# Optimization experiments

Hardware: AMD Instinct MI355X
Metric: run time of the kernel (lower is better)

## Reference

```python
import jax, jax.numpy as jnp
import numpy as np

EPS = 1e-5

def _layernorm(x, g, b):
    mu = x.mean(-1, keepdims=True)
    var = ((x - mu) ** 2).mean(-1, keepdims=True)
    return (x - mu) * jax.lax.rsqrt(var + EPS) * g + b

def setup_inputs() -> dict:
    key = jax.random.key(0)
    ks = jax.random.split(key, 8)
    T, TOK, E = 16, 16384, 128
    N_NODE, NUM_NODES = 8192, 50000
    COMP_LEN, MAX_LEN, COMP_DIM = 64, 782, 32
    return {
        "x": jax.random.normal(ks[0], (T, TOK, E), jnp.float32),
        "ln1_g": jax.random.normal(ks[1], (E,), jnp.float32),
        "ln1_b": jax.random.normal(ks[2], (E,), jnp.float32),
        "ln2_g": jax.random.normal(ks[3], (COMP_LEN * COMP_DIM,), jnp.float32),
        "ln2_b": jax.random.normal(ks[4], (COMP_LEN * COMP_DIM,), jnp.float32),
        "node_idx": jax.random.randint(ks[5], (T, N_NODE), 0, NUM_NODES),
        "stacked_indices": jax.random.randint(ks[6], (COMP_LEN, MAX_LEN), 0, NUM_NODES),
        "n_node": N_NODE,
        "num_nodes": NUM_NODES,
    }

def reference(x, ln1_g, ln1_b, ln2_g, ln2_b, node_idx, stacked_indices, n_node, num_nodes):
    T, TOK, E = x.shape
    comp_len, max_len = stacked_indices.shape
    comp_dim = ln2_g.shape[0] // comp_len
    # encode_layer_norm over embed_dim
    xn = _layernorm(x, ln1_g, ln1_b)
    # node tokens occupy the first n_node token slots (padded_node_mask)
    nodes = xn[:, :n_node, :]                              # [T, n_node, E]
    # scga._to_entire: scatter-add per-timestamp node embeds to entire-node tensor
    flat_idx = (jnp.arange(T)[:, None] * num_nodes + node_idx).reshape(-1)
    tee = jax.ops.segment_sum(nodes.reshape(-1, E), flat_idx,
                              num_segments=T * num_nodes)
    tee = tee.reshape(T, num_nodes, E)                     # [T, N, E]
    # AdaptiveAvgPool1d(comp_dim): exact block mean since E % comp_dim == 0
    pooled = tee.reshape(T, num_nodes, comp_dim, E // comp_dim).mean(-1)  # [T, N, C]
    # basket gather + mean over basket slots
    gath = pooled[:, stacked_indices, :]                   # [T, comp_len, max_len, C]
    agg = gath.sum(2) / max_len                            # [T, comp_len, C]
    compressed = agg.reshape(T, 1, comp_len * comp_dim)
    return _layernorm(compressed, ln2_g, ln2_b)
```

## Files before the change

kernel.cpp:

```cpp
#include <hip/hip_runtime.h>
#include <hip/hip_cooperative_groups.h>

namespace cg = cooperative_groups;

constexpr int T_DIM       = 16;
constexpr int TOK         = 16384;
constexpr int E_DIM       = 128;
constexpr int N_NODE_C    = 8192;
constexpr int NUM_NODES_C = 50000;
constexpr int COMP_LEN_C  = 64;
constexpr int MAX_LEN_C   = 782;
constexpr int COMP_DIM_C  = 32;
constexpr float EPS_F     = 1e-5f;

constexpr int D2      = COMP_LEN_C * COMP_DIM_C;
constexpr int GRID_C  = 1024;
constexpr int BLK_C   = 256;
constexpr int PER_T   = 64;
constexpr int RPB     = 128;
constexpr int W_WORDS = NUM_NODES_C * COMP_LEN_C / 4;

constexpr size_t W8_BYTES = (size_t)NUM_NODES_C * COMP_LEN_C;
constexpr size_t P_OFF    = 3211264;
constexpr size_t AGG_OFF  = P_OFF + (size_t)T_DIM * PER_T * D2 * 4;

struct SharedT {
  float    vtile[RPB][COMP_DIM_C];
  unsigned atile[RPB][16];
  float    red[256];
};

__device__ __forceinline__ void phase_main(
    SharedT& sh, int bid, const float* __restrict__ x, const float* __restrict__ g1,
    const float* __restrict__ b1, const int* __restrict__ node_idx,
    const unsigned* __restrict__ W32, float* __restrict__ P) {
  const int t = bid >> 6, chunk = bid & 63;
  const int tid = threadIdx.x, lane = tid & 63, wave = tid >> 6;
  const int g = lane & 31, half = lane >> 5;
  const int rbase = chunk * RPB;
  const int* nit = node_idx + (size_t)t * N_NODE_C;
  const float4* xv = reinterpret_cast<const float4*>(x + (size_t)t * TOK * E_DIM);

  int nid8[8];
#pragma unroll
  for (int j = 0; j < 8; ++j) nid8[j] = nit[rbase + ((tid + j * 256) >> 4)];

  const float4 gv = *reinterpret_cast<const float4*>(g1 + g * 4);
  const float4 bv = *reinterpret_cast<const float4*>(b1 + g * 4);
  const float sg = gv.x + gv.y + gv.z + gv.w;
  const float sb = bv.x + bv.y + bv.z + bv.w;
  const int wr0 = rbase + wave * 32;

  float4 xd[8];
#pragma unroll
  for (int i = 0; i < 8; ++i)
    xd[i] = xv[(size_t)(wr0 + 2 * i) * 32 + lane];

  unsigned wg8[8];
#pragma unroll
  for (int j = 0; j < 8; ++j)
    wg8[j] = W32[(size_t)nid8[j] * 16 + ((tid + j * 256) & 15)];

#pragma unroll
  for (int i = 0; i < 8; ++i) {
    const float4 a = xd[i];
    float s = (a.x + a.y) + (a.z + a.w);
    float q = a.x * a.x + a.y * a.y + a.z * a.z + a.w * a.w;
#pragma unroll
    for (int m = 1; m < 32; m <<= 1) { s += __shfl_xor(s, m); q += __shfl_xor(q, m); }
    float mu = s * (1.0f / E_DIM);
    float rstd = rsqrtf(q * (1.0f / E_DIM) - mu * mu + EPS_F);
    float dxg = a.x * gv.x + a.y * gv.y + a.z * gv.z + a.w * gv.w;
    sh.vtile[wave * 32 + 2 * i + half][g] = (dxg - mu * sg) * rstd + sb;
  }
#pragma unroll
  for (int i = 0; i < 8; ++i)
    xd[i] = xv[(size_t)(wr0 + 16 + 2 * i) * 32 + lane];
#pragma unroll
  for (int j = 0; j < 8; ++j) {
    int w = tid + j * 256;
    sh.atile[w >> 4][w & 15] = wg8[j];
  }
#pragma unroll
  for (int i = 0; i < 8; ++i) {
    const float4 a = xd[i];
    float s = (a.x + a.y) + (a.z + a.w);
    float q = a.x * a.x + a.y * a.y + a.z * a.z + a.w * a.w;
#pragma unroll
    for (int m = 1; m < 32; m <<= 1) { s += __shfl_xor(s, m); q += __shfl_xor(q, m); }
    float mu = s * (1.0f / E_DIM);
    float rstd = rsqrtf(q * (1.0f / E_DIM) - mu * mu + EPS_F);
    float dxg = a.x * gv.x + a.y * gv.y + a.z * gv.z + a.w * gv.w;
    sh.vtile[wave * 32 + 16 + 2 * i + half][g] = (dxg - mu * sg) * rstd + sb;
  }
  __syncthreads();

  const int c4 = tid >> 4, d2 = tid & 15;
  float2 acc0{0,0}, acc1{0,0}, acc2{0,0}, acc3{0,0};
  const float2* vt2 = reinterpret_cast<const float2*>(&sh.vtile[0][0]);
#pragma unroll 4
  for (int k = 0; k < RPB; ++k) {
    unsigned a4 = sh.atile[k][c4];
    float2 v2 = vt2[k * 16 + d2];
    float a0 = (float)(a4 & 255u),         a1 = (float)((a4 >> 8) & 255u);
    float a2 = (float)((a4 >> 16) & 255u), a3 = (float)((a4 >> 24) & 255u);
    acc0.x += a0 * v2.x; acc0.y += a0 * v2.y;
    acc1.x += a1 * v2.x; acc1.y += a1 * v2.y;
    acc2.x += a2 * v2.x; acc2.y += a2 * v2.y;
    acc3.x += a3 * v2.x; acc3.y += a3 * v2.y;
  }
  float2* pr2 = reinterpret_cast<float2*>(P + ((size_t)t * PER_T + chunk) * D2);
  pr2[(c4 * 4 + 0) * 16 + d2] = acc0;
  pr2[(c4 * 4 + 1) * 16 + d2] = acc1;
  pr2[(c4 * 4 + 2) * 16 + d2] = acc2;
  pr2[(c4 * 4 + 3) * 16 + d2] = acc3;
}

__device__ __forceinline__ void phase_reduce(
    SharedT& sh, int b, const float* __restrict__ P, float* __restrict__ Agg) {
  const int t = b >> 5, seg = b & 31;
  const int tid = threadIdx.x;
  const int elem = seg * 64 + (tid & 63);
  const int q = tid >> 6;
  const float* base = P + (size_t)t * PER_T * D2 + elem;
  float acc = 0.f;
#pragma unroll
  for (int p = 0; p < 16; ++p) acc += base[(size_t)(q * 16 + p) * D2];
  sh.red[tid] = acc;
  __syncthreads();
  if (tid < 64)
    Agg[(size_t)t * D2 + elem] =
        sh.red[tid] + sh.red[tid + 64] + sh.red[tid + 128] + sh.red[tid + 192];
}

__device__ __forceinline__ void phase_final(
    SharedT& sh, int t, const float* __restrict__ Agg, const float* __restrict__ g2,
    const float* __restrict__ b2, float* __restrict__ out) {
  const float scale = 1.0f / (4.0f * (float)MAX_LEN_C);
  const int tid = threadIdx.x;
  float y[8]; float s = 0.f, q = 0.f;
#pragma unroll
  for (int k = 0; k < 8; ++k) {
    float v = Agg[(size_t)t * D2 + tid * 8 + k] * scale;
    y[k] = v; s += v; q += v * v;
  }
#pragma unroll
  for (int m = 1; m < 64; m <<= 1) { s += __shfl_xor(s, m); q += __shfl_xor(q, m); }
  const int w = tid >> 6, ln = tid & 63;
  if (ln == 0) { sh.red[w] = s; sh.red[8 + w] = q; }
  __syncthreads();
  float ts = sh.red[0] + sh.red[1] + sh.red[2] + sh.red[3];
  float tq = sh.red[8] + sh.red[9] + sh.red[10] + sh.red[11];
  float mu = ts * (1.0f / D2);
  float rstd = rsqrtf(tq * (1.0f / D2) - mu * mu + EPS_F);
#pragma unroll
  for (int k = 0; k < 8; ++k) {
    int idx = tid * 8 + k;
    out[(size_t)t * D2 + idx] = (y[k] - mu) * rstd * g2[idx] + b2[idx];
  }
}

__global__ __launch_bounds__(256, 4) void mega_kernel(
    const float* __restrict__ x, const float* __restrict__ g1, const float* __restrict__ b1,
    const int* __restrict__ node_idx, const int* __restrict__ sidx,
    const float* __restrict__ g2, const float* __restrict__ b2,
    unsigned* __restrict__ W8w, float* __restrict__ P, float* __restrict__ Agg,
    float* __restrict__ out) {
  cg::grid_group grid = cg::this_grid();
  __shared__ SharedT sh;
  const int gtid = blockIdx.x * BLK_C + threadIdx.x;

  for (int i = gtid; i < W_WORDS; i += GRID_C * BLK_C) W8w[i] = 0u;
  grid.sync();
  if (gtid < COMP_LEN_C * MAX_LEN_C) {
    int c = gtid / MAX_LEN_C;
    int n = sidx[gtid];
    int byteoff = n * COMP_LEN_C + c;
    atomicAdd(&W8w[byteoff >> 2], 1u << (8 * (byteoff & 3)));
  }
  grid.sync();
  phase_main(sh, blockIdx.x, x, g1, b1, node_idx, (const unsigned*)W8w, P);
  grid.sync();
  if (blockIdx.x < 512) phase_reduce(sh, blockIdx.x, P, Agg);
  grid.sync();
  if (blockIdx.x < T_DIM) phase_final(sh, blockIdx.x, Agg, g2, b2, out);
}

__global__ void build_w8_kernel(const int* __restrict__ sidx, unsigned* __restrict__ W8w) {
  const int c  = blockIdx.x >> 2;
  const int jc = blockIdx.x & 3;
  const int j  = jc * 196 + threadIdx.x;
  if (j < MAX_LEN_C && threadIdx.x < 196) {
    int n = sidx[c * MAX_LEN_C + j];
    int byteoff = n * COMP_LEN_C + c;
    atomicAdd(&W8w[byteoff >> 2], 1u << (8 * (byteoff & 3)));
  }
}
__global__ __launch_bounds__(256, 4) void main_nc(
    const float* __restrict__ x, const float* __restrict__ g1, const float* __restrict__ b1,
    const int* __restrict__ node_idx, const unsigned* __restrict__ W32,
    float* __restrict__ P) {
  __shared__ SharedT sh;
  phase_main(sh, blockIdx.x, x, g1, b1, node_idx, W32, P);
}
__global__ __launch_bounds__(256) void reduce_nc(const float* __restrict__ P,
                                                float* __restrict__ Agg) {
  __shared__ SharedT sh;
  phase_reduce(sh, blockIdx.x, P, Agg);
}
__global__ __launch_bounds__(256) void final_nc(
    const float* __restrict__ Agg, const float* __restrict__ g2,
    const float* __restrict__ b2, float* __restrict__ out) {
  __shared__ SharedT sh;
  phase_final(sh, blockIdx.x, Agg, g2, b2, out);
}

extern "C" void kernel_launch(void* const* d_in, const int* in_sizes, int n_in,
                              void* d_out, int out_size, void* d_ws, size_t ws_size,
                              hipStream_t stream) {
  const float* x     = (const float*)d_in[0];
  const float* ln1_g = (const float*)d_in[1];
  const float* ln1_b = (const float*)d_in[2];
  const float* ln2_g = (const float*)d_in[3];
  const float* ln2_b = (const float*)d_in[4];
  const int* node_idx = (const int*)d_in[5];
  const int* sidx     = (const int*)d_in[6];
  float* out = (float*)d_out;

  unsigned char* ws = (unsigned char*)d_ws;
  unsigned* W8w = (unsigned*)ws;
  float* P   = (float*)(ws + P_OFF);
  float* Agg = (float*)(ws + AGG_OFF);

  int maxActive = 0;
  hipError_t occ = hipOccupancyMaxActiveBlocksPerMultiprocessor(
      &maxActive, (const void*)mega_kernel, BLK_C, 0);
  bool coop = (occ == hipSuccess) && (maxActive >= 4);

  if (coop) {
    void* args[] = {(void*)&x, (void*)&ln1_g, (void*)&ln1_b, (void*)&node_idx,
                    (void*)&sidx, (void*)&ln2_g, (void*)&ln2_b,
                    (void*)&W8w, (void*)&P, (void*)&Agg, (void*)&out};
    hipError_t e = hipLaunchCooperativeKernel((void*)mega_kernel, dim3(GRID_C),
                                              dim3(BLK_C), args, 0, stream);
    if (e == hipSuccess) return;
  }

  hipMemsetAsync(W8w, 0, W8_BYTES, stream);
  build_w8_kernel<<<COMP_LEN_C * 4, 256, 0, stream>>>(sidx, W8w);
  main_nc<<<GRID_C, BLK_C, 0, stream>>>(x, ln1_g, ln1_b, node_idx,
                                        (const unsigned*)W8w, P);
  reduce_nc<<<512, 256, 0, stream>>>(P, Agg);
  final_nc<<<T_DIM, 256, 0, stream>>>(Agg, ln2_g, ln2_b, out);
}
```

Measured before the change: 43.46 us.

## Overlap LN streaming with weight build, atomically accumulate partials, drop reduce phase

The layernorm streaming of x now runs before the first grid sync, so it overlaps with building the basket count table. Per-block partial sums are added straight into the per-timestamp aggregate with float atomics, which removes the partial buffer, the separate reduce phase and one grid sync. Zeroing of the count table and aggregate moves from in-kernel stores to a host-issued memset before the launch. The cost is atomic contention (64 blocks per timestamp add into the same 2048 floats), nondeterministic float summation order, and an extra memset operation on the stream.

```diff
diff --git a/kernel.cpp b/kernel.cpp
--- a/kernel.cpp
+++ b/kernel.cpp
@@ -18,30 +18,28 @@
 constexpr int BLK_C   = 256;
 constexpr int PER_T   = 64;
 constexpr int RPB     = 128;
-constexpr int W_WORDS = NUM_NODES_C * COMP_LEN_C / 4;
-
-constexpr size_t W8_BYTES = (size_t)NUM_NODES_C * COMP_LEN_C;
-constexpr size_t P_OFF    = 3211264;
-constexpr size_t AGG_OFF  = P_OFF + (size_t)T_DIM * PER_T * D2 * 4;
+
+constexpr size_t W8_BYTES   = (size_t)NUM_NODES_C * COMP_LEN_C;
+constexpr size_t AGG_OFF    = 3211264;
+constexpr size_t AGG_BYTES  = (size_t)T_DIM * D2 * sizeof(float);
+constexpr size_t ZERO_BYTES = AGG_OFF + AGG_BYTES;
 
 struct SharedT {
   float    vtile[RPB][COMP_DIM_C];
   unsigned atile[RPB][16];
-  float    red[256];
+  float    red[16];
 };
 
-__device__ __forceinline__ void phase_main(
-    SharedT& sh, int bid, const float* __restrict__ x, const float* __restrict__ g1,
-    const float* __restrict__ b1, const int* __restrict__ node_idx,
-    const unsigned* __restrict__ W32, float* __restrict__ P) {
-  const int t = bid >> 6, chunk = bid & 63;
+__device__ __forceinline__ void phaseA_stream(
+    SharedT& sh, int t, int chunk, const float* __restrict__ x,
+    const float* __restrict__ g1, const float* __restrict__ b1,
+    const int* __restrict__ node_idx, int* nid8) {
   const int tid = threadIdx.x, lane = tid & 63, wave = tid >> 6;
   const int g = lane & 31, half = lane >> 5;
   const int rbase = chunk * RPB;
   const int* nit = node_idx + (size_t)t * N_NODE_C;
   const float4* xv = reinterpret_cast<const float4*>(x + (size_t)t * TOK * E_DIM);
 
-  int nid8[8];
 #pragma unroll
   for (int j = 0; j < 8; ++j) nid8[j] = nit[rbase + ((tid + j * 256) >> 4)];
 
@@ -55,12 +53,6 @@
 #pragma unroll
   for (int i = 0; i < 8; ++i)
     xd[i] = xv[(size_t)(wr0 + 2 * i) * 32 + lane];
-
-  unsigned wg8[8];
-#pragma unroll
-  for (int j = 0; j < 8; ++j)
-    wg8[j] = W32[(size_t)nid8[j] * 16 + ((tid + j * 256) & 15)];
-
 #pragma unroll
   for (int i = 0; i < 8; ++i) {
     const float4 a = xd[i];
@@ -77,11 +69,6 @@
   for (int i = 0; i < 8; ++i)
     xd[i] = xv[(size_t)(wr0 + 16 + 2 * i) * 32 + lane];
 #pragma unroll
-  for (int j = 0; j < 8; ++j) {
-    int w = tid + j * 256;
-    sh.atile[w >> 4][w & 15] = wg8[j];
-  }
-#pragma unroll
   for (int i = 0; i < 8; ++i) {
     const float4 a = xd[i];
     float s = (a.x + a.y) + (a.z + a.w);
@@ -92,6 +79,23 @@
     float rstd = rsqrtf(q * (1.0f / E_DIM) - mu * mu + EPS_F);
     float dxg = a.x * gv.x + a.y * gv.y + a.z * gv.z + a.w * gv.w;
     sh.vtile[wave * 32 + 16 + 2 * i + half][g] = (dxg - mu * sg) * rstd + sb;
+  }
+}
+
+__device__ __forceinline__ void phaseB_gemmflush(
+    SharedT& sh, int t, const unsigned* __restrict__ W32, const int* nid8,
+    float* __restrict__ Agg) {
+  const int tid = threadIdx.x;
+  __syncthreads();
+
+  unsigned wg8[8];
+#pragma unroll
+  for (int j = 0; j < 8; ++j)
+    wg8[j] = W32[(size_t)nid8[j] * 16 + ((tid + j * 256) & 15)];
+#pragma unroll
+  for (int j = 0; j < 8; ++j) {
+    int w = tid + j * 256;
+    sh.atile[w >> 4][w & 15] = wg8[j];
   }
   __syncthreads();
 
@@ -109,31 +113,19 @@
     acc2.x += a2 * v2.x; acc2.y += a2 * v2.y;
     acc3.x += a3 * v2.x; acc3.y += a3 * v2.y;
   }
-  float2* pr2 = reinterpret_cast<float2*>(P + ((size_t)t * PER_T + chunk) * D2);
-  pr2[(c4 * 4 + 0) * 16 + d2] = acc0;
-  pr2[(c4 * 4 + 1) * 16 + d2] = acc1;
-  pr2[(c4 * 4 + 2) * 16 + d2] = acc2;
-  pr2[(c4 * 4 + 3) * 16 + d2] = acc3;
-}
-
-__device__ __forceinline__ void phase_reduce(
-    SharedT& sh, int b, const float* __restrict__ P, float* __restrict__ Agg) {
-  const int t = b >> 5, seg = b & 31;
-  const int tid = threadIdx.x;
-  const int elem = seg * 64 + (tid & 63);
-  const int q = tid >> 6;
-  const float* base = P + (size_t)t * PER_T * D2 + elem;
-  float acc = 0.f;
-#pragma unroll
-  for (int p = 0; p < 16; ++p) acc += base[(size_t)(q * 16 + p) * D2];
-  sh.red[tid] = acc;
-  __syncthreads();
-  if (tid < 64)
-    Agg[(size_t)t * D2 + elem] =
-        sh.red[tid] + sh.red[tid + 64] + sh.red[tid + 128] + sh.red[tid + 192];
-}
-
-__device__ __forceinline__ void phase_final(
+  float* aggt = Agg + (size_t)t * D2;
+  const int b0 = c4 * 4;
+  atomicAdd(&aggt[(b0 + 0) * 32 + d2 * 2],     acc0.x);
+  atomicAdd(&aggt[(b0 + 0) * 32 + d2 * 2 + 1], acc0.y);
+  atomicAdd(&aggt[(b0 + 1) * 32 + d2 * 2],     acc1.x);
+  atomicAdd(&aggt[(b0 + 1) * 32 + d2 * 2 + 1], acc1.y);
+  atomicAdd(&aggt[(b0 + 2) * 32 + d2 * 2],     acc2.x);
+  atomicAdd(&aggt[(b0 + 2) * 32 + d2 * 2 + 1], acc2.y);
+  atomicAdd(&aggt[(b0 + 3) * 32 + d2 * 2],     acc3.x);
+  atomicAdd(&aggt[(b0 + 3) * 32 + d2 * 2 + 1], acc3.y);
+}
+
+__device__ __forceinline__ void phaseC_final(
     SharedT& sh, int t, const float* __restrict__ Agg, const float* __restrict__ g2,
     const float* __restrict__ b2, float* __restrict__ out) {
   const float scale = 1.0f / (4.0f * (float)MAX_LEN_C);
@@ -164,26 +156,24 @@
     const float* __restrict__ x, const float* __restrict__ g1, const float* __restrict__ b1,
     const int* __restrict__ node_idx, const int* __restrict__ sidx,
     const float* __restrict__ g2, const float* __restrict__ b2,
-    unsigned* __restrict__ W8w, float* __restrict__ P, float* __restrict__ Agg,
-    float* __restrict__ out) {
+    unsigned* __restrict__ W8w, float* __restrict__ Agg, float* __restrict__ out) {
   cg::grid_group grid = cg::this_grid();
   __shared__ SharedT sh;
   const int gtid = blockIdx.x * BLK_C + threadIdx.x;
-
-  for (int i = gtid; i < W_WORDS; i += GRID_C * BLK_C) W8w[i] = 0u;
-  grid.sync();
+  const int t = blockIdx.x >> 6, chunk = blockIdx.x & 63;
+
   if (gtid < COMP_LEN_C * MAX_LEN_C) {
     int c = gtid / MAX_LEN_C;
     int n = sidx[gtid];
     int byteoff = n * COMP_LEN_C + c;
     atomicAdd(&W8w[byteoff >> 2], 1u << (8 * (byteoff & 3)));
   }
+  int nid8[8];
+  phaseA_stream(sh, t, chunk, x, g1, b1, node_idx, nid8);
   grid.sync();
-  phase_main(sh, blockIdx.x, x, g1, b1, node_idx, (const unsigned*)W8w, P);
+  phaseB_gemmflush(sh, t, (const unsigned*)W8w, nid8, Agg);
   grid.sync();
-  if (blockIdx.x < 512) phase_reduce(sh, blockIdx.x, P, Agg);
-  grid.sync();
-  if (blockIdx.x < T_DIM) phase_final(sh, blockIdx.x, Agg, g2, b2, out);
+  if (blockIdx.x < T_DIM) phaseC_final(sh, blockIdx.x, Agg, g2, b2, out);
 }
 
 __global__ void build_w8_kernel(const int* __restrict__ sidx, unsigned* __restrict__ W8w) {
@@ -199,20 +189,18 @@
 __global__ __launch_bounds__(256, 4) void main_nc(
     const float* __restrict__ x, const float* __restrict__ g1, const float* __restrict__ b1,
     const int* __restrict__ node_idx, const unsigned* __restrict__ W32,
-    float* __restrict__ P) {
+    float* __restrict__ Agg) {
   __shared__ SharedT sh;
-  phase_main(sh, blockIdx.x, x, g1, b1, node_idx, W32, P);
-}
-__global__ __launch_bounds__(256) void reduce_nc(const float* __restrict__ P,
-                                                float* __restrict__ Agg) {
-  __shared__ SharedT sh;
-  phase_reduce(sh, blockIdx.x, P, Agg);
+  const int t = blockIdx.x >> 6, chunk = blockIdx.x & 63;
+  int nid8[8];
+  phaseA_stream(sh, t, chunk, x, g1, b1, node_idx, nid8);
+  phaseB_gemmflush(sh, t, W32, nid8, Agg);
 }
 __global__ __launch_bounds__(256) void final_nc(
     const float* __restrict__ Agg, const float* __restrict__ g2,
     const float* __restrict__ b2, float* __restrict__ out) {
   __shared__ SharedT sh;
-  phase_final(sh, blockIdx.x, Agg, g2, b2, out);
+  phaseC_final(sh, blockIdx.x, Agg, g2, b2, out);
 }
 
 extern "C" void kernel_launch(void* const* d_in, const int* in_sizes, int n_in,
@@ -229,8 +217,9 @@
 
   unsigned char* ws = (unsigned char*)d_ws;
   unsigned* W8w = (unsigned*)ws;
-  float* P   = (float*)(ws + P_OFF);
   float* Agg = (float*)(ws + AGG_OFF);
+
+  hipMemsetAsync(ws, 0, ZERO_BYTES, stream);
 
   int maxActive = 0;
   hipError_t occ = hipOccupancyMaxActiveBlocksPerMultiprocessor(
@@ -240,16 +229,14 @@
   if (coop) {
     void* args[] = {(void*)&x, (void*)&ln1_g, (void*)&ln1_b, (void*)&node_idx,
                     (void*)&sidx, (void*)&ln2_g, (void*)&ln2_b,
-                    (void*)&W8w, (void*)&P, (void*)&Agg, (void*)&out};
+                    (void*)&W8w, (void*)&Agg, (void*)&out};
     hipError_t e = hipLaunchCooperativeKernel((void*)mega_kernel, dim3(GRID_C),
                                               dim3(BLK_C), args, 0, stream);
     if (e == hipSuccess) return;
   }
 
-  hipMemsetAsync(W8w, 0, W8_BYTES, stream);
   build_w8_kernel<<<COMP_LEN_C * 4, 256, 0, stream>>>(sidx, W8w);
   main_nc<<<GRID_C, BLK_C, 0, stream>>>(x, ln1_g, ln1_b, node_idx,
-                                        (const unsigned*)W8w, P);
-  reduce_nc<<<512, 256, 0, stream>>>(P, Agg);
+                                        (const unsigned*)W8w, Agg);
   final_nc<<<T_DIM, 256, 0, stream>>>(Agg, ln2_g, ln2_b, out);
 }
```

After: 45.00 us. +3.6%, slower.
